# Optimization experiments

Hardware: AMD Instinct MI355X
Metric: run time of the kernel (lower is better)

## Reference

```python
import jax, jax.numpy as jnp
import numpy as np

B, C, N = 8, 768, 256
H = 12            # num_heads[0]
D = C // H        # head_dim = 64


def setup_inputs() -> dict:
    key = jax.random.key(0)
    ks = jax.random.split(key, 4)
    s = 0.02
    return {
        "x_ori": jax.random.normal(ks[0], (B, C, N), jnp.float32),
        "cross": jax.random.normal(ks[1], (B, C, N), jnp.float32),
        "W_proj": jax.random.normal(ks[2], (C, C), jnp.float32) * s,
        "b_proj": jnp.zeros((C,), jnp.float32),
        "W_dep": jax.random.normal(ks[3], (C, C), jnp.float32) * s,
        "b_dep": jnp.zeros((C,), jnp.float32),
    }


def reference(x_ori, cross, W_proj, b_proj, W_dep, b_dep):
    # x_ori, cross: [B, C, N] with channel axis factored as (head_dim D, num_heads H)
    Bn, Cn, Nn = x_ori.shape
    Nc = cross.shape[-1]
    scale = D ** (-0.5)

    # 'B (d H) N -> B d (H N)'
    x = x_ori.reshape(Bn, D, H, Nn).reshape(Bn, D, H * Nn)

    # proj over channel axis (1x1 conv): [B, C, Nc]
    cp = jnp.einsum('oc,bcn->bon', W_proj, cross) + b_proj[None, :, None]
    cp = cp.reshape(Bn, D, H, Nc).reshape(Bn, D, H * Nc)      # 'B (d H) Nc -> B d (H Nc)'

    # 'B (d H) Nc -> B (H Nc) d'
    cr = cross.reshape(Bn, D, H, Nc).transpose(0, 2, 3, 1).reshape(Bn, H * Nc, D)

    # raw attention (no softmax in original source)
    atten = jnp.einsum('bdm,bdn->bmn', x, cp) * scale          # [B, H*N, H*Nc]
    out = jnp.einsum('bmn,bnd->bmd', atten, cr)                # [B, H*N, D]

    # 'B (N H) d -> B N (H d)'  (note (num, head) grouping per source)
    out = out.reshape(Bn, Nn, H, D).reshape(Bn, Nn, H * D)

    y = out @ W_dep.T + b_dep                                  # deproj: [B, N, C]
    # skip connection (dropout is identity at eval / drop_ratio=0)
    return x_ori + y.transpose(0, 2, 1)
```

## Files before the change

kernel.cpp:

```cpp
#include <hip/hip_runtime.h>

typedef unsigned short u16;
typedef short bf16x8 __attribute__((ext_vector_type(8)));
typedef float f32x4 __attribute__((ext_vector_type(4)));

#define BB 8
#define CC 768
#define NN 256
#define HH 12
#define DD 64
#define K3 3072
#define BCN 196608
#define SCALE 0.125f
#define LDP 72

__device__ __forceinline__ u16 f2b(float f) {
    union { float f; unsigned int i; } v; v.f = f;
    unsigned int r = v.i + 0x7FFFu + ((v.i >> 16) & 1u);
    return (u16)(r >> 16);
}

__global__ __launch_bounds__(256) void k_proj(
    const float* __restrict__ Wp, const float* __restrict__ cross,
    const float* __restrict__ bp, u16* __restrict__ cp, float* __restrict__ G)
{
    __shared__ __align__(16) u16 As[64 * LDP];
    __shared__ __align__(16) u16 Bs[64 * LDP];
    __shared__ __align__(16) float T[64][68];
    const int n0 = blockIdx.x * 64;
    const int o0 = blockIdx.y * 64;
    const int b  = blockIdx.z;
    const int t = threadIdx.x;
    const int lane = t & 63, wave = t >> 6;
    const int q = lane >> 4, tx = lane & 15;
    const int wm = (wave & 1) * 32, wn = (wave >> 1) * 32;

    if (blockIdx.x == 0 && blockIdx.y == 0) {
        float4 z = {0.f, 0.f, 0.f, 0.f};
        float* Gb = G + b * 4096;
        #pragma unroll
        for (int j = 0; j < 4; ++j)
            *reinterpret_cast<float4*>(Gb + t * 4 + j * 1024) = z;
    }

    const float* crb = cross + b * BCN;
    f32x4 acc[2][2] = {};
    for (int c0 = 0; c0 < CC; c0 += 64) {
        {
            const int r = t >> 2, cq = t & 3;
            const float* src = Wp + (o0 + r) * CC + c0;
            u16* dst = As + r * LDP;
            #pragma unroll
            for (int u = 0; u < 4; ++u) {
                const int cl = (cq + 4 * u) * 4;
                float4 v = *reinterpret_cast<const float4*>(src + cl);
                ushort4 w; w.x = f2b(v.x); w.y = f2b(v.y); w.z = f2b(v.z); w.w = f2b(v.w);
                *reinterpret_cast<ushort4*>(dst + cl) = w;
            }
        }
        {
            const int r = t >> 2, fq = t & 3;
            const float* src = crb + (c0 + r) * NN + n0;
            #pragma unroll
            for (int u = 0; u < 4; ++u) {
                const int nl = (fq + 4 * u) * 4;
                float4 v = *reinterpret_cast<const float4*>(src + nl);
                T[r][nl + 0] = v.x; T[r][nl + 1] = v.y; T[r][nl + 2] = v.z; T[r][nl + 3] = v.w;
            }
        }
        __syncthreads();
        {
            const int nn = t >> 2, cq = t & 3;
            u16* dst = Bs + nn * LDP;
            #pragma unroll
            for (int u = 0; u < 4; ++u) {
                const int c4 = (cq + 4 * u) * 4;
                ushort4 w;
                w.x = f2b(T[c4 + 0][nn]); w.y = f2b(T[c4 + 1][nn]);
                w.z = f2b(T[c4 + 2][nn]); w.w = f2b(T[c4 + 3][nn]);
                *reinterpret_cast<ushort4*>(dst + c4) = w;
            }
        }
        __syncthreads();
        #pragma unroll
        for (int kk = 0; kk < 2; ++kk) {
            bf16x8 a0 = *reinterpret_cast<bf16x8*>(As + (wm + tx) * LDP + kk * 32 + q * 8);
            bf16x8 a1 = *reinterpret_cast<bf16x8*>(As + (wm + 16 + tx) * LDP + kk * 32 + q * 8);
            bf16x8 b0 = *reinterpret_cast<bf16x8*>(Bs + (wn + tx) * LDP + kk * 32 + q * 8);
            bf16x8 b1 = *reinterpret_cast<bf16x8*>(Bs + (wn + 16 + tx) * LDP + kk * 32 + q * 8);
            acc[0][0] = __builtin_amdgcn_mfma_f32_16x16x32_bf16(a0, b0, acc[0][0], 0, 0, 0);
            acc[0][1] = __builtin_amdgcn_mfma_f32_16x16x32_bf16(a0, b1, acc[0][1], 0, 0, 0);
            acc[1][0] = __builtin_amdgcn_mfma_f32_16x16x32_bf16(a1, b0, acc[1][0], 0, 0, 0);
            acc[1][1] = __builtin_amdgcn_mfma_f32_16x16x32_bf16(a1, b1, acc[1][1], 0, 0, 0);
        }
        __syncthreads();
    }
    u16* cpb = cp + b * BCN;
    #pragma unroll
    for (int i = 0; i < 2; ++i)
        #pragma unroll
        for (int j = 0; j < 2; ++j)
            #pragma unroll
            for (int r = 0; r < 4; ++r) {
                const int o = o0 + wm + i * 16 + q * 4 + r;
                const int n = n0 + wn + j * 16 + tx;
                cpb[o * NN + n] = f2b(acc[i][j][r] + bp[o]);
            }
}

__global__ __launch_bounds__(256) void k_gram(
    const float* __restrict__ cross, const u16* __restrict__ cp, float* __restrict__ G)
{
    __shared__ __align__(16) u16 As[64 * LDP];
    __shared__ __align__(16) u16 Bs[64 * LDP];
    const int kb = blockIdx.x * 64;
    const int b  = blockIdx.y;
    const int t = threadIdx.x;
    const int lane = t & 63, wave = t >> 6;
    const int q = lane >> 4, tx = lane & 15;
    const int wm = (wave & 1) * 32, wn = (wave >> 1) * 32;
    const float* crb = cross + b * BCN;
    const u16* cpb = cp + b * BCN;
    f32x4 acc[2][2] = {};
    {
        const int r = t >> 2, cq = t & 3;
        const float* src = crb + r * K3 + kb;
        u16* dst = As + r * LDP;
        #pragma unroll
        for (int u = 0; u < 4; ++u) {
            const int cl = (cq + 4 * u) * 4;
            float4 v = *reinterpret_cast<const float4*>(src + cl);
            ushort4 w; w.x = f2b(v.x); w.y = f2b(v.y); w.z = f2b(v.z); w.w = f2b(v.w);
            *reinterpret_cast<ushort4*>(dst + cl) = w;
        }
    }
    {
        const int r = t >> 3, ch = (t & 7) * 8;
        *reinterpret_cast<uint4*>(Bs + r * LDP + ch) =
            *reinterpret_cast<const uint4*>(cpb + r * K3 + kb + ch);
        *reinterpret_cast<uint4*>(Bs + (r + 32) * LDP + ch) =
            *reinterpret_cast<const uint4*>(cpb + (r + 32) * K3 + kb + ch);
    }
    __syncthreads();
    #pragma unroll
    for (int kk = 0; kk < 2; ++kk) {
        bf16x8 a0 = *reinterpret_cast<bf16x8*>(As + (wm + tx) * LDP + kk * 32 + q * 8);
        bf16x8 a1 = *reinterpret_cast<bf16x8*>(As + (wm + 16 + tx) * LDP + kk * 32 + q * 8);
        bf16x8 b0 = *reinterpret_cast<bf16x8*>(Bs + (wn + tx) * LDP + kk * 32 + q * 8);
        bf16x8 b1 = *reinterpret_cast<bf16x8*>(Bs + (wn + 16 + tx) * LDP + kk * 32 + q * 8);
        acc[0][0] = __builtin_amdgcn_mfma_f32_16x16x32_bf16(a0, b0, acc[0][0], 0, 0, 0);
        acc[0][1] = __builtin_amdgcn_mfma_f32_16x16x32_bf16(a0, b1, acc[0][1], 0, 0, 0);
        acc[1][0] = __builtin_amdgcn_mfma_f32_16x16x32_bf16(a1, b0, acc[1][0], 0, 0, 0);
        acc[1][1] = __builtin_amdgcn_mfma_f32_16x16x32_bf16(a1, b1, acc[1][1], 0, 0, 0);
    }
    float* Gb = G + b * 4096;
    #pragma unroll
    for (int i = 0; i < 2; ++i)
        #pragma unroll
        for (int j = 0; j < 2; ++j)
            #pragma unroll
            for (int r = 0; r < 4; ++r) {
                const int dd = wm + i * 16 + q * 4 + r;
                const int d  = wn + j * 16 + tx;
                atomicAdd(Gb + dd * DD + d, acc[i][j][r] * SCALE);
            }
}

__global__ __launch_bounds__(256) void k_xm(
    const float* __restrict__ x, const float* __restrict__ G, u16* __restrict__ U)
{
    __shared__ __align__(16) u16 As[64 * LDP];
    __shared__ __align__(16) u16 Bs[64 * LDP];
    __shared__ __align__(16) float T[64][68];
    const int m0 = blockIdx.x * 64;
    const int b  = blockIdx.y;
    const int h   = m0 >> 8;
    const int nn0 = m0 & 255;
    const int t = threadIdx.x;
    const int lane = t & 63, wave = t >> 6;
    const int q = lane >> 4, tx = lane & 15;
    const int wm = (wave & 1) * 32, wn = (wave >> 1) * 32;
    const float* xb = x + b * BCN;
    const float* Gb = G + b * 4096;
    f32x4 acc[2][2] = {};
    {
        const int d = t >> 2, fq = t & 3;
        const float* src = xb + (d * HH + h) * NN + nn0;
        #pragma unroll
        for (int u = 0; u < 4; ++u) {
            const int nl = (fq + 4 * u) * 4;
            float4 v = *reinterpret_cast<const float4*>(src + nl);
            T[d][nl + 0] = v.x; T[d][nl + 1] = v.y; T[d][nl + 2] = v.z; T[d][nl + 3] = v.w;
        }
    }
    {
        const int r = t >> 2, cq = t & 3;
        const float* src = Gb + r * DD;
        u16* dst = Bs + r * LDP;
        #pragma unroll
        for (int u = 0; u < 4; ++u) {
            const int cl = (cq + 4 * u) * 4;
            float4 v = *reinterpret_cast<const float4*>(src + cl);
            ushort4 w; w.x = f2b(v.x); w.y = f2b(v.y); w.z = f2b(v.z); w.w = f2b(v.w);
            *reinterpret_cast<ushort4*>(dst + cl) = w;
        }
    }
    __syncthreads();
    {
        const int nn = t >> 2, dq = t & 3;
        u16* dst = As + nn * LDP;
        #pragma unroll
        for (int u = 0; u < 4; ++u) {
            const int d4 = (dq + 4 * u) * 4;
            ushort4 w;
            w.x = f2b(T[d4 + 0][nn]); w.y = f2b(T[d4 + 1][nn]);
            w.z = f2b(T[d4 + 2][nn]); w.w = f2b(T[d4 + 3][nn]);
            *reinterpret_cast<ushort4*>(dst + d4) = w;
        }
    }
    __syncthreads();
    #pragma unroll
    for (int kk = 0; kk < 2; ++kk) {
        bf16x8 a0 = *reinterpret_cast<bf16x8*>(As + (wm + tx) * LDP + kk * 32 + q * 8);
        bf16x8 a1 = *reinterpret_cast<bf16x8*>(As + (wm + 16 + tx) * LDP + kk * 32 + q * 8);
        bf16x8 b0 = *reinterpret_cast<bf16x8*>(Bs + (wn + tx) * LDP + kk * 32 + q * 8);
        bf16x8 b1 = *reinterpret_cast<bf16x8*>(Bs + (wn + 16 + tx) * LDP + kk * 32 + q * 8);
        acc[0][0] = __builtin_amdgcn_mfma_f32_16x16x32_bf16(a0, b0, acc[0][0], 0, 0, 0);
        acc[0][1] = __builtin_amdgcn_mfma_f32_16x16x32_bf16(a0, b1, acc[0][1], 0, 0, 0);
        acc[1][0] = __builtin_amdgcn_mfma_f32_16x16x32_bf16(a1, b0, acc[1][0], 0, 0, 0);
        acc[1][1] = __builtin_amdgcn_mfma_f32_16x16x32_bf16(a1, b1, acc[1][1], 0, 0, 0);
    }
    u16* Ub = U + b * BCN;
    #pragma unroll
    for (int i = 0; i < 2; ++i)
        #pragma unroll
        for (int j = 0; j < 2; ++j)
            #pragma unroll
            for (int r = 0; r < 4; ++r) {
                const int m  = m0 + wm + i * 16 + q * 4 + r;
                const int dd = wn + j * 16 + tx;
                Ub[m * DD + dd] = f2b(acc[i][j][r]);
            }
}

__global__ __launch_bounds__(256) void k_dep(
    const float* __restrict__ Wd, const u16* __restrict__ U,
    const float* __restrict__ bd, const float* __restrict__ x, float* __restrict__ out)
{
    __shared__ __align__(16) u16 As[64 * LDP];
    __shared__ __align__(16) u16 Bs[64 * LDP];
    const int n0 = blockIdx.x * 64;
    const int o0 = blockIdx.y * 64;
    const int b  = blockIdx.z;
    const int t = threadIdx.x;
    const int lane = t & 63, wave = t >> 6;
    const int q = lane >> 4, tx = lane & 15;
    const int wm = (wave & 1) * 32, wn = (wave >> 1) * 32;
    const u16* Ub = U + b * BCN;
    f32x4 acc[2][2] = {};
    for (int c0 = 0; c0 < CC; c0 += 64) {
        {
            const int r = t >> 2, cq = t & 3;
            const float* src = Wd + (o0 + r) * CC + c0;
            u16* dst = As + r * LDP;
            #pragma unroll
            for (int u = 0; u < 4; ++u) {
                const int cl = (cq + 4 * u) * 4;
                float4 v = *reinterpret_cast<const float4*>(src + cl);
                ushort4 w; w.x = f2b(v.x); w.y = f2b(v.y); w.z = f2b(v.z); w.w = f2b(v.w);
                *reinterpret_cast<ushort4*>(dst + cl) = w;
            }
        }
        {
            const int r = t >> 3, ch = (t & 7) * 8;
            *reinterpret_cast<uint4*>(Bs + r * LDP + ch) =
                *reinterpret_cast<const uint4*>(Ub + (n0 + r) * CC + c0 + ch);
            *reinterpret_cast<uint4*>(Bs + (r + 32) * LDP + ch) =
                *reinterpret_cast<const uint4*>(Ub + (n0 + r + 32) * CC + c0 + ch);
        }
        __syncthreads();
        #pragma unroll
        for (int kk = 0; kk < 2; ++kk) {
            bf16x8 a0 = *reinterpret_cast<bf16x8*>(As + (wm + tx) * LDP + kk * 32 + q * 8);
            bf16x8 a1 = *reinterpret_cast<bf16x8*>(As + (wm + 16 + tx) * LDP + kk * 32 + q * 8);
            bf16x8 b0 = *reinterpret_cast<bf16x8*>(Bs + (wn + tx) * LDP + kk * 32 + q * 8);
            bf16x8 b1 = *reinterpret_cast<bf16x8*>(Bs + (wn + 16 + tx) * LDP + kk * 32 + q * 8);
            acc[0][0] = __builtin_amdgcn_mfma_f32_16x16x32_bf16(a0, b0, acc[0][0], 0, 0, 0);
            acc[0][1] = __builtin_amdgcn_mfma_f32_16x16x32_bf16(a0, b1, acc[0][1], 0, 0, 0);
            acc[1][0] = __builtin_amdgcn_mfma_f32_16x16x32_bf16(a1, b0, acc[1][0], 0, 0, 0);
            acc[1][1] = __builtin_amdgcn_mfma_f32_16x16x32_bf16(a1, b1, acc[1][1], 0, 0, 0);
        }
        __syncthreads();
    }
    #pragma unroll
    for (int i = 0; i < 2; ++i)
        #pragma unroll
        for (int j = 0; j < 2; ++j)
            #pragma unroll
            for (int r = 0; r < 4; ++r) {
                const int o = o0 + wm + i * 16 + q * 4 + r;
                const int n = n0 + wn + j * 16 + tx;
                const int idx = b * BCN + o * NN + n;
                out[idx] = acc[i][j][r] + bd[o] + x[idx];
            }
}

extern "C" void kernel_launch(void* const* d_in, const int* in_sizes, int n_in,
                              void* d_out, int out_size, void* d_ws, size_t ws_size,
                              hipStream_t stream) {
    const float* x_ori = (const float*)d_in[0];
    const float* cross = (const float*)d_in[1];
    const float* Wp    = (const float*)d_in[2];
    const float* bp    = (const float*)d_in[3];
    const float* Wd    = (const float*)d_in[4];
    const float* bd    = (const float*)d_in[5];
    float* out = (float*)d_out;

    u16*   cp = (u16*)d_ws;
    u16*   U  = (u16*)d_ws;
    float* G  = (float*)((char*)d_ws + (size_t)BB * BCN * sizeof(u16));

    k_proj<<<dim3(4, 12, BB), 256, 0, stream>>>(Wp, cross, bp, cp, G);
    k_gram<<<dim3(48, BB), 256, 0, stream>>>(cross, cp, G);
    k_xm  <<<dim3(48, BB), 256, 0, stream>>>(x_ori, G, U);
    k_dep <<<dim3(4, 12, BB), 256, 0, stream>>>(Wd, U, bd, x_ori, out);
}
```

Measured before the change: 124.8 us.

## Reassociate Gram via cross self-covariance and split-K deproj with atomics

Replaces the projection-then-Gram pipeline with a per-batch cross covariance S = cross·crossᵀ (768x768 with K=256), then forms the head Gram by contracting W_proj against S, adding the bias term through row sums of cross. The x transpose and bf16 conversion is folded into the first kernel, and the output is initialised with x + b_dep inside the xm kernel. Deproj is split along K into two halves that atomically accumulate into the output. This trades the K=768 projection GEMM for a smaller S GEMM plus a strided W_proj GEMM, but adds a 9.4MB bf16 S intermediate and float atomics on the output.

```diff
diff --git a/kernel.cpp b/kernel.cpp
--- a/kernel.cpp
+++ b/kernel.cpp
@@ -9,8 +9,8 @@
 #define NN 256
 #define HH 12
 #define DD 64
-#define K3 3072
 #define BCN 196608
+#define SWS 589824
 #define SCALE 0.125f
 #define LDP 72
 
@@ -20,66 +20,157 @@
     return (u16)(r >> 16);
 }
 
-__global__ __launch_bounds__(256) void k_proj(
-    const float* __restrict__ Wp, const float* __restrict__ cross,
-    const float* __restrict__ bp, u16* __restrict__ cp, float* __restrict__ G)
+
+__global__ __launch_bounds__(256) void k_S(
+    const float* __restrict__ cross, const float* __restrict__ x,
+    u16* __restrict__ S, u16* __restrict__ xT,
+    float* __restrict__ G, float* __restrict__ R)
 {
-    __shared__ __align__(16) u16 As[64 * LDP];
-    __shared__ __align__(16) u16 Bs[64 * LDP];
-    __shared__ __align__(16) float T[64][68];
-    const int n0 = blockIdx.x * 64;
-    const int o0 = blockIdx.y * 64;
-    const int b  = blockIdx.z;
-    const int t = threadIdx.x;
+    __shared__ __align__(16) u16 SMEM[2 * 64 * LDP];
+    u16* As = SMEM;
+    u16* Bs = SMEM + 64 * LDP;
+    float (*T)[68] = reinterpret_cast<float(*)[68]>(SMEM);
+    const int b = blockIdx.y, blk = blockIdx.x, t = threadIdx.x;
     const int lane = t & 63, wave = t >> 6;
     const int q = lane >> 4, tx = lane & 15;
     const int wm = (wave & 1) * 32, wn = (wave >> 1) * 32;
 
-    if (blockIdx.x == 0 && blockIdx.y == 0) {
-        float4 z = {0.f, 0.f, 0.f, 0.f};
-        float* Gb = G + b * 4096;
-        #pragma unroll
-        for (int j = 0; j < 4; ++j)
-            *reinterpret_cast<float4*>(Gb + t * 4 + j * 1024) = z;
-    }
-
-    const float* crb = cross + b * BCN;
+    if (blk < 144) {
+        const int r0 = (blk / 12) * 64, c0 = (blk % 12) * 64;
+        const float* crb = cross + b * BCN;
+        f32x4 acc[2][2] = {};
+        for (int k4 = 0; k4 < 4; ++k4) {
+            const int nk = k4 * 64;
+            {
+                const int r = t >> 2, q4 = t & 3;
+                const float* sa = crb + (r0 + r) * NN + nk;
+                const float* sb = crb + (c0 + r) * NN + nk;
+                u16* da = As + r * LDP;
+                u16* db = Bs + r * LDP;
+                #pragma unroll
+                for (int u = 0; u < 4; ++u) {
+                    const int cl = (q4 + 4 * u) * 4;
+                    float4 va = *reinterpret_cast<const float4*>(sa + cl);
+                    float4 vb = *reinterpret_cast<const float4*>(sb + cl);
+                    ushort4 wa, wb;
+                    wa.x = f2b(va.x); wa.y = f2b(va.y); wa.z = f2b(va.z); wa.w = f2b(va.w);
+                    wb.x = f2b(vb.x); wb.y = f2b(vb.y); wb.z = f2b(vb.z); wb.w = f2b(vb.w);
+                    *reinterpret_cast<ushort4*>(da + cl) = wa;
+                    *reinterpret_cast<ushort4*>(db + cl) = wb;
+                }
+            }
+            __syncthreads();
+            #pragma unroll
+            for (int kk = 0; kk < 2; ++kk) {
+                bf16x8 a0 = *reinterpret_cast<bf16x8*>(As + (wm + tx) * LDP + kk * 32 + q * 8);
+                bf16x8 a1 = *reinterpret_cast<bf16x8*>(As + (wm + 16 + tx) * LDP + kk * 32 + q * 8);
+                bf16x8 b0 = *reinterpret_cast<bf16x8*>(Bs + (wn + tx) * LDP + kk * 32 + q * 8);
+                bf16x8 b1 = *reinterpret_cast<bf16x8*>(Bs + (wn + 16 + tx) * LDP + kk * 32 + q * 8);
+                acc[0][0] = __builtin_amdgcn_mfma_f32_16x16x32_bf16(a0, b0, acc[0][0], 0, 0, 0);
+                acc[0][1] = __builtin_amdgcn_mfma_f32_16x16x32_bf16(a0, b1, acc[0][1], 0, 0, 0);
+                acc[1][0] = __builtin_amdgcn_mfma_f32_16x16x32_bf16(a1, b0, acc[1][0], 0, 0, 0);
+                acc[1][1] = __builtin_amdgcn_mfma_f32_16x16x32_bf16(a1, b1, acc[1][1], 0, 0, 0);
+            }
+            __syncthreads();
+        }
+        u16* Sb = S + b * SWS;
+        #pragma unroll
+        for (int i = 0; i < 2; ++i)
+            #pragma unroll
+            for (int j = 0; j < 2; ++j)
+                #pragma unroll
+                for (int r = 0; r < 4; ++r) {
+                    const int row = r0 + wm + i * 16 + q * 4 + r;
+                    const int col = c0 + wn + j * 16 + tx;
+                    Sb[row * CC + col] = f2b(acc[i][j][r]);
+                }
+        if (blk == 0) {
+            float4 z = {0.f, 0.f, 0.f, 0.f};
+            float* Gb = G + b * 4096;
+            #pragma unroll
+            for (int u = 0; u < 4; ++u)
+                *reinterpret_cast<float4*>(Gb + t * 16 + u * 4) = z;
+        }
+        if (r0 == c0) {
+            float* Rp = (float*)As;
+            const int row = t >> 2, seg = t & 3;
+            const float* src = crb + (r0 + row) * NN + seg * 64;
+            float s = 0.f;
+            #pragma unroll
+            for (int u = 0; u < 16; ++u) {
+                float4 v = *reinterpret_cast<const float4*>(src + u * 4);
+                s += v.x + v.y + v.z + v.w;
+            }
+            Rp[t] = s;
+            __syncthreads();
+            if (t < 64)
+                R[b * CC + r0 + t] = Rp[t * 4] + Rp[t * 4 + 1] + Rp[t * 4 + 2] + Rp[t * 4 + 3];
+        }
+    } else {
+        const int idx = blk - 144;
+        const int m0 = idx * 64, h = m0 >> 8, nn0 = m0 & 255;
+        const float* xb = x + b * BCN;
+        {
+            const int d = t >> 2, fq = t & 3;
+            const float* src = xb + (d * HH + h) * NN + nn0;
+            #pragma unroll
+            for (int u = 0; u < 4; ++u) {
+                const int nl = (fq + 4 * u) * 4;
+                float4 v = *reinterpret_cast<const float4*>(src + nl);
+                T[d][nl + 0] = v.x; T[d][nl + 1] = v.y; T[d][nl + 2] = v.z; T[d][nl + 3] = v.w;
+            }
+        }
+        __syncthreads();
+        {
+            const int nn = t >> 2, dq = t & 3;
+            u16* dst = xT + b * BCN + (m0 + nn) * DD;
+            #pragma unroll
+            for (int u = 0; u < 4; ++u) {
+                const int d4 = (dq + 4 * u) * 4;
+                ushort4 w;
+                w.x = f2b(T[d4 + 0][nn]); w.y = f2b(T[d4 + 1][nn]);
+                w.z = f2b(T[d4 + 2][nn]); w.w = f2b(T[d4 + 3][nn]);
+                *reinterpret_cast<ushort4*>(dst + d4) = w;
+            }
+        }
+    }
+}
+
+__global__ __launch_bounds__(256) void k_g(
+    const float* __restrict__ Wp, const u16* __restrict__ S,
+    const float* __restrict__ bp, const float* __restrict__ R,
+    float* __restrict__ G)
+{
+    __shared__ __align__(16) u16 SMEM[2 * 64 * LDP];
+    u16* As = SMEM;
+    u16* Bs = SMEM + 64 * LDP;
+    const int b = blockIdx.y, kc = blockIdx.x, t = threadIdx.x;
+    const int j = kc >> 1, cb = (kc & 1) * 384;
+    const int lane = t & 63, wave = t >> 6;
+    const int q = lane >> 4, tx = lane & 15;
+    const int wm = (wave & 1) * 32, wn = (wave >> 1) * 32;
+    const u16* Sb = S + b * SWS;
     f32x4 acc[2][2] = {};
-    for (int c0 = 0; c0 < CC; c0 += 64) {
-        {
-            const int r = t >> 2, cq = t & 3;
-            const float* src = Wp + (o0 + r) * CC + c0;
+    for (int ii = 0; ii < 6; ++ii) {
+        const int c0 = cb + ii * 64;
+        {
+            const int r = t >> 2, q4 = t & 3;
+            const float* src = Wp + (r * HH + j) * CC + c0;
             u16* dst = As + r * LDP;
             #pragma unroll
             for (int u = 0; u < 4; ++u) {
-                const int cl = (cq + 4 * u) * 4;
+                const int cl = (q4 + 4 * u) * 4;
                 float4 v = *reinterpret_cast<const float4*>(src + cl);
                 ushort4 w; w.x = f2b(v.x); w.y = f2b(v.y); w.z = f2b(v.z); w.w = f2b(v.w);
                 *reinterpret_cast<ushort4*>(dst + cl) = w;
             }
         }
         {
-            const int r = t >> 2, fq = t & 3;
-            const float* src = crb + (c0 + r) * NN + n0;
-            #pragma unroll
-            for (int u = 0; u < 4; ++u) {
-                const int nl = (fq + 4 * u) * 4;
-                float4 v = *reinterpret_cast<const float4*>(src + nl);
-                T[r][nl + 0] = v.x; T[r][nl + 1] = v.y; T[r][nl + 2] = v.z; T[r][nl + 3] = v.w;
-            }
-        }
-        __syncthreads();
-        {
-            const int nn = t >> 2, cq = t & 3;
-            u16* dst = Bs + nn * LDP;
-            #pragma unroll
-            for (int u = 0; u < 4; ++u) {
-                const int c4 = (cq + 4 * u) * 4;
-                ushort4 w;
-                w.x = f2b(T[c4 + 0][nn]); w.y = f2b(T[c4 + 1][nn]);
-                w.z = f2b(T[c4 + 2][nn]); w.w = f2b(T[c4 + 3][nn]);
-                *reinterpret_cast<ushort4*>(dst + c4) = w;
-            }
+            const int r = t >> 3, ch = (t & 7) * 8;
+            *reinterpret_cast<uint4*>(Bs + r * LDP + ch) =
+                *reinterpret_cast<const uint4*>(Sb + (r * HH + j) * CC + c0 + ch);
+            *reinterpret_cast<uint4*>(Bs + (r + 32) * LDP + ch) =
+                *reinterpret_cast<const uint4*>(Sb + ((r + 32) * HH + j) * CC + c0 + ch);
         }
         __syncthreads();
         #pragma unroll
@@ -95,188 +186,80 @@
         }
         __syncthreads();
     }
-    u16* cpb = cp + b * BCN;
-    #pragma unroll
-    for (int i = 0; i < 2; ++i)
-        #pragma unroll
-        for (int j = 0; j < 2; ++j)
-            #pragma unroll
-            for (int r = 0; r < 4; ++r) {
-                const int o = o0 + wm + i * 16 + q * 4 + r;
-                const int n = n0 + wn + j * 16 + tx;
-                cpb[o * NN + n] = f2b(acc[i][j][r] + bp[o]);
-            }
-}
-
-__global__ __launch_bounds__(256) void k_gram(
-    const float* __restrict__ cross, const u16* __restrict__ cp, float* __restrict__ G)
+    float* Gb = G + b * 4096;
+    if (kc == 0) {
+        float* bpf = (float*)As;
+        float* Rf  = bpf + CC;
+        #pragma unroll
+        for (int u = 0; u < 3; ++u) {
+            const int idx = t + u * 256;
+            bpf[idx] = bp[idx];
+            Rf[idx]  = R[b * CC + idx];
+        }
+        __syncthreads();
+        #pragma unroll
+        for (int i = 0; i < 2; ++i)
+            #pragma unroll
+            for (int j2 = 0; j2 < 2; ++j2)
+                #pragma unroll
+                for (int r = 0; r < 4; ++r) {
+                    const int dI  = wm + i * 16 + q * 4 + r;
+                    const int ddI = wn + j2 * 16 + tx;
+                    float bias = 0.f;
+                    #pragma unroll
+                    for (int jj = 0; jj < HH; ++jj)
+                        bias += bpf[dI * HH + jj] * Rf[ddI * HH + jj];
+                    atomicAdd(Gb + ddI * DD + dI, SCALE * (acc[i][j2][r] + bias));
+                }
+    } else {
+        #pragma unroll
+        for (int i = 0; i < 2; ++i)
+            #pragma unroll
+            for (int j2 = 0; j2 < 2; ++j2)
+                #pragma unroll
+                for (int r = 0; r < 4; ++r) {
+                    const int dI  = wm + i * 16 + q * 4 + r;
+                    const int ddI = wn + j2 * 16 + tx;
+                    atomicAdd(Gb + ddI * DD + dI, SCALE * acc[i][j2][r]);
+                }
+    }
+}
+
+__global__ __launch_bounds__(256) void k_xm2(
+    const u16* __restrict__ xT, const float* __restrict__ G,
+    const float* __restrict__ x, const float* __restrict__ bd,
+    u16* __restrict__ U, float* __restrict__ out)
 {
-    __shared__ __align__(16) u16 As[64 * LDP];
-    __shared__ __align__(16) u16 Bs[64 * LDP];
-    const int kb = blockIdx.x * 64;
-    const int b  = blockIdx.y;
-    const int t = threadIdx.x;
-    const int lane = t & 63, wave = t >> 6;
-    const int q = lane >> 4, tx = lane & 15;
-    const int wm = (wave & 1) * 32, wn = (wave >> 1) * 32;
-    const float* crb = cross + b * BCN;
-    const u16* cpb = cp + b * BCN;
-    f32x4 acc[2][2] = {};
-    {
-        const int r = t >> 2, cq = t & 3;
-        const float* src = crb + r * K3 + kb;
-        u16* dst = As + r * LDP;
-        #pragma unroll
-        for (int u = 0; u < 4; ++u) {
-            const int cl = (cq + 4 * u) * 4;
-            float4 v = *reinterpret_cast<const float4*>(src + cl);
-            ushort4 w; w.x = f2b(v.x); w.y = f2b(v.y); w.z = f2b(v.z); w.w = f2b(v.w);
-            *reinterpret_cast<ushort4*>(dst + cl) = w;
-        }
-    }
-    {
-        const int r = t >> 3, ch = (t & 7) * 8;
-        *reinterpret_cast<uint4*>(Bs + r * LDP + ch) =
-            *reinterpret_cast<const uint4*>(cpb + r * K3 + kb + ch);
-        *reinterpret_cast<uint4*>(Bs + (r + 32) * LDP + ch) =
-            *reinterpret_cast<const uint4*>(cpb + (r + 32) * K3 + kb + ch);
-    }
-    __syncthreads();
-    #pragma unroll
-    for (int kk = 0; kk < 2; ++kk) {
-        bf16x8 a0 = *reinterpret_cast<bf16x8*>(As + (wm + tx) * LDP + kk * 32 + q * 8);
-        bf16x8 a1 = *reinterpret_cast<bf16x8*>(As + (wm + 16 + tx) * LDP + kk * 32 + q * 8);
-        bf16x8 b0 = *reinterpret_cast<bf16x8*>(Bs + (wn + tx) * LDP + kk * 32 + q * 8);
-        bf16x8 b1 = *reinterpret_cast<bf16x8*>(Bs + (wn + 16 + tx) * LDP + kk * 32 + q * 8);
-        acc[0][0] = __builtin_amdgcn_mfma_f32_16x16x32_bf16(a0, b0, acc[0][0], 0, 0, 0);
-        acc[0][1] = __builtin_amdgcn_mfma_f32_16x16x32_bf16(a0, b1, acc[0][1], 0, 0, 0);
-        acc[1][0] = __builtin_amdgcn_mfma_f32_16x16x32_bf16(a1, b0, acc[1][0], 0, 0, 0);
-        acc[1][1] = __builtin_amdgcn_mfma_f32_16x16x32_bf16(a1, b1, acc[1][1], 0, 0, 0);
-    }
-    float* Gb = G + b * 4096;
-    #pragma unroll
-    for (int i = 0; i < 2; ++i)
-        #pragma unroll
-        for (int j = 0; j < 2; ++j)
-            #pragma unroll
-            for (int r = 0; r < 4; ++r) {
-                const int dd = wm + i * 16 + q * 4 + r;
-                const int d  = wn + j * 16 + tx;
-                atomicAdd(Gb + dd * DD + d, acc[i][j][r] * SCALE);
-            }
-}
-
-__global__ __launch_bounds__(256) void k_xm(
-    const float* __restrict__ x, const float* __restrict__ G, u16* __restrict__ U)
-{
-    __shared__ __align__(16) u16 As[64 * LDP];
-    __shared__ __align__(16) u16 Bs[64 * LDP];
-    __shared__ __align__(16) float T[64][68];
-    const int m0 = blockIdx.x * 64;
-    const int b  = blockIdx.y;
-    const int h   = m0 >> 8;
-    const int nn0 = m0 & 255;
-    const int t = threadIdx.x;
-    const int lane = t & 63, wave = t >> 6;
-    const int q = lane >> 4, tx = lane & 15;
-    const int wm = (wave & 1) * 32, wn = (wave >> 1) * 32;
-    const float* xb = x + b * BCN;
-    const float* Gb = G + b * 4096;
-    f32x4 acc[2][2] = {};
-    {
-        const int d = t >> 2, fq = t & 3;
-        const float* src = xb + (d * HH + h) * NN + nn0;
-        #pragma unroll
-        for (int u = 0; u < 4; ++u) {
-            const int nl = (fq + 4 * u) * 4;
-            float4 v = *reinterpret_cast<const float4*>(src + nl);
-            T[d][nl + 0] = v.x; T[d][nl + 1] = v.y; T[d][nl + 2] = v.z; T[d][nl + 3] = v.w;
-        }
-    }
-    {
-        const int r = t >> 2, cq = t & 3;
-        const float* src = Gb + r * DD;
-        u16* dst = Bs + r * LDP;
-        #pragma unroll
-        for (int u = 0; u < 4; ++u) {
-            const int cl = (cq + 4 * u) * 4;
-            float4 v = *reinterpret_cast<const float4*>(src + cl);
-            ushort4 w; w.x = f2b(v.x); w.y = f2b(v.y); w.z = f2b(v.z); w.w = f2b(v.w);
-            *reinterpret_cast<ushort4*>(dst + cl) = w;
-        }
-    }
-    __syncthreads();
-    {
-        const int nn = t >> 2, dq = t & 3;
-        u16* dst = As + nn * LDP;
-        #pragma unroll
-        for (int u = 0; u < 4; ++u) {
-            const int d4 = (dq + 4 * u) * 4;
-            ushort4 w;
-            w.x = f2b(T[d4 + 0][nn]); w.y = f2b(T[d4 + 1][nn]);
-            w.z = f2b(T[d4 + 2][nn]); w.w = f2b(T[d4 + 3][nn]);
-            *reinterpret_cast<ushort4*>(dst + d4) = w;
-        }
-    }
-    __syncthreads();
-    #pragma unroll
-    for (int kk = 0; kk < 2; ++kk) {
-        bf16x8 a0 = *reinterpret_cast<bf16x8*>(As + (wm + tx) * LDP + kk * 32 + q * 8);
-        bf16x8 a1 = *reinterpret_cast<bf16x8*>(As + (wm + 16 + tx) * LDP + kk * 32 + q * 8);
-        bf16x8 b0 = *reinterpret_cast<bf16x8*>(Bs + (wn + tx) * LDP + kk * 32 + q * 8);
-        bf16x8 b1 = *reinterpret_cast<bf16x8*>(Bs + (wn + 16 + tx) * LDP + kk * 32 + q * 8);
-        acc[0][0] = __builtin_amdgcn_mfma_f32_16x16x32_bf16(a0, b0, acc[0][0], 0, 0, 0);
-        acc[0][1] = __builtin_amdgcn_mfma_f32_16x16x32_bf16(a0, b1, acc[0][1], 0, 0, 0);
-        acc[1][0] = __builtin_amdgcn_mfma_f32_16x16x32_bf16(a1, b0, acc[1][0], 0, 0, 0);
-        acc[1][1] = __builtin_amdgcn_mfma_f32_16x16x32_bf16(a1, b1, acc[1][1], 0, 0, 0);
-    }
-    u16* Ub = U + b * BCN;
-    #pragma unroll
-    for (int i = 0; i < 2; ++i)
-        #pragma unroll
-        for (int j = 0; j < 2; ++j)
-            #pragma unroll
-            for (int r = 0; r < 4; ++r) {
-                const int m  = m0 + wm + i * 16 + q * 4 + r;
-                const int dd = wn + j * 16 + tx;
-                Ub[m * DD + dd] = f2b(acc[i][j][r]);
-            }
-}
-
-__global__ __launch_bounds__(256) void k_dep(
-    const float* __restrict__ Wd, const u16* __restrict__ U,
-    const float* __restrict__ bd, const float* __restrict__ x, float* __restrict__ out)
-{
-    __shared__ __align__(16) u16 As[64 * LDP];
-    __shared__ __align__(16) u16 Bs[64 * LDP];
-    const int n0 = blockIdx.x * 64;
-    const int o0 = blockIdx.y * 64;
-    const int b  = blockIdx.z;
-    const int t = threadIdx.x;
-    const int lane = t & 63, wave = t >> 6;
-    const int q = lane >> 4, tx = lane & 15;
-    const int wm = (wave & 1) * 32, wn = (wave >> 1) * 32;
-    const u16* Ub = U + b * BCN;
-    f32x4 acc[2][2] = {};
-    for (int c0 = 0; c0 < CC; c0 += 64) {
-        {
-            const int r = t >> 2, cq = t & 3;
-            const float* src = Wd + (o0 + r) * CC + c0;
-            u16* dst = As + r * LDP;
-            #pragma unroll
-            for (int u = 0; u < 4; ++u) {
-                const int cl = (cq + 4 * u) * 4;
+    __shared__ __align__(16) u16 SMEM[2 * 64 * LDP];
+    u16* As = SMEM;
+    u16* Bs = SMEM + 64 * LDP;
+    const int b = blockIdx.y, blk = blockIdx.x, t = threadIdx.x;
+    if (blk < 48) {
+        const int m0 = blk * 64;
+        const int lane = t & 63, wave = t >> 6;
+        const int q = lane >> 4, tx = lane & 15;
+        const int wm = (wave & 1) * 32, wn = (wave >> 1) * 32;
+        const u16* xTb = xT + b * BCN;
+        const float* Gb = G + b * 4096;
+        f32x4 acc[2][2] = {};
+        {
+            const int r = t >> 3, ch = (t & 7) * 8;
+            *reinterpret_cast<uint4*>(As + r * LDP + ch) =
+                *reinterpret_cast<const uint4*>(xTb + (m0 + r) * DD + ch);
+            *reinterpret_cast<uint4*>(As + (r + 32) * LDP + ch) =
+                *reinterpret_cast<const uint4*>(xTb + (m0 + r + 32) * DD + ch);
+        }
+        {
+            const int r = t >> 2, q4 = t & 3;
+            const float* src = Gb + r * DD;
+            u16* dst = Bs + r * LDP;
+            #pragma unroll
+            for (int u = 0; u < 4; ++u) {
+                const int cl = (q4 + 4 * u) * 4;
                 float4 v = *reinterpret_cast<const float4*>(src + cl);
                 ushort4 w; w.x = f2b(v.x); w.y = f2b(v.y); w.z = f2b(v.z); w.w = f2b(v.w);
                 *reinterpret_cast<ushort4*>(dst + cl) = w;
             }
-        }
-        {
-            const int r = t >> 3, ch = (t & 7) * 8;
-            *reinterpret_cast<uint4*>(Bs + r * LDP + ch) =
-                *reinterpret_cast<const uint4*>(Ub + (n0 + r) * CC + c0 + ch);
-            *reinterpret_cast<uint4*>(Bs + (r + 32) * LDP + ch) =
-                *reinterpret_cast<const uint4*>(Ub + (n0 + r + 32) * CC + c0 + ch);
         }
         __syncthreads();
         #pragma unroll
@@ -290,6 +273,80 @@
             acc[1][0] = __builtin_amdgcn_mfma_f32_16x16x32_bf16(a1, b0, acc[1][0], 0, 0, 0);
             acc[1][1] = __builtin_amdgcn_mfma_f32_16x16x32_bf16(a1, b1, acc[1][1], 0, 0, 0);
         }
+        u16* Ub = U + b * BCN;
+        #pragma unroll
+        for (int i = 0; i < 2; ++i)
+            #pragma unroll
+            for (int j = 0; j < 2; ++j)
+                #pragma unroll
+                for (int r = 0; r < 4; ++r) {
+                    const int m  = m0 + wm + i * 16 + q * 4 + r;
+                    const int dd = wn + j * 16 + tx;
+                    Ub[m * DD + dd] = f2b(acc[i][j][r]);
+                }
+    } else {
+        const int idx = blk - 48;
+        const int base = b * BCN + idx * 4096 + t * 16;
+        #pragma unroll
+        for (int u = 0; u < 4; ++u) {
+            const int off = idx * 4096 + t * 16 + u * 4;
+            const int o = off >> 8;
+            float4 v = *reinterpret_cast<const float4*>(x + base + u * 4);
+            const float bb = bd[o];
+            v.x += bb; v.y += bb; v.z += bb; v.w += bb;
+            *reinterpret_cast<float4*>(out + base + u * 4) = v;
+        }
+    }
+}
+
+__global__ __launch_bounds__(256) void k_dep(
+    const float* __restrict__ Wd, const u16* __restrict__ U, float* __restrict__ out)
+{
+    __shared__ __align__(16) u16 As[64 * LDP];
+    __shared__ __align__(16) u16 Bs[64 * LDP];
+    const int n0 = blockIdx.x * 64;
+    const int o0 = blockIdx.y * 64;
+    const int b  = blockIdx.z >> 1;
+    const int cb = (blockIdx.z & 1) * 384;
+    const int t = threadIdx.x;
+    const int lane = t & 63, wave = t >> 6;
+    const int q = lane >> 4, tx = lane & 15;
+    const int wm = (wave & 1) * 32, wn = (wave >> 1) * 32;
+    const u16* Ub = U + b * BCN;
+    f32x4 acc[2][2] = {};
+    for (int ii = 0; ii < 6; ++ii) {
+        const int c0 = cb + ii * 64;
+        {
+            const int r = t >> 2, q4 = t & 3;
+            const float* src = Wd + (o0 + r) * CC + c0;
+            u16* dst = As + r * LDP;
+            #pragma unroll
+            for (int u = 0; u < 4; ++u) {
+                const int cl = (q4 + 4 * u) * 4;
+                float4 v = *reinterpret_cast<const float4*>(src + cl);
+                ushort4 w; w.x = f2b(v.x); w.y = f2b(v.y); w.z = f2b(v.z); w.w = f2b(v.w);
+                *reinterpret_cast<ushort4*>(dst + cl) = w;
+            }
+        }
+        {
+            const int r = t >> 3, ch = (t & 7) * 8;
+            *reinterpret_cast<uint4*>(Bs + r * LDP + ch) =
+                *reinterpret_cast<const uint4*>(Ub + (n0 + r) * CC + c0 + ch);
+            *reinterpret_cast<uint4*>(Bs + (r + 32) * LDP + ch) =
+                *reinterpret_cast<const uint4*>(Ub + (n0 + r + 32) * CC + c0 + ch);
+        }
+        __syncthreads();
+        #pragma unroll
+        for (int kk = 0; kk < 2; ++kk) {
+            bf16x8 a0 = *reinterpret_cast<bf16x8*>(As + (wm + tx) * LDP + kk * 32 + q * 8);
+            bf16x8 a1 = *reinterpret_cast<bf16x8*>(As + (wm + 16 + tx) * LDP + kk * 32 + q * 8);
+            bf16x8 b0 = *reinterpret_cast<bf16x8*>(Bs + (wn + tx) * LDP + kk * 32 + q * 8);
+            bf16x8 b1 = *reinterpret_cast<bf16x8*>(Bs + (wn + 16 + tx) * LDP + kk * 32 + q * 8);
+            acc[0][0] = __builtin_amdgcn_mfma_f32_16x16x32_bf16(a0, b0, acc[0][0], 0, 0, 0);
+            acc[0][1] = __builtin_amdgcn_mfma_f32_16x16x32_bf16(a0, b1, acc[0][1], 0, 0, 0);
+            acc[1][0] = __builtin_amdgcn_mfma_f32_16x16x32_bf16(a1, b0, acc[1][0], 0, 0, 0);
+            acc[1][1] = __builtin_amdgcn_mfma_f32_16x16x32_bf16(a1, b1, acc[1][1], 0, 0, 0);
+        }
         __syncthreads();
     }
     #pragma unroll
@@ -300,8 +357,7 @@
             for (int r = 0; r < 4; ++r) {
                 const int o = o0 + wm + i * 16 + q * 4 + r;
                 const int n = n0 + wn + j * 16 + tx;
-                const int idx = b * BCN + o * NN + n;
-                out[idx] = acc[i][j][r] + bd[o] + x[idx];
+                atomicAdd(out + b * BCN + o * NN + n, acc[i][j][r]);
             }
 }
 
@@ -316,12 +372,15 @@
     const float* bd    = (const float*)d_in[5];
     float* out = (float*)d_out;
 
-    u16*   cp = (u16*)d_ws;
-    u16*   U  = (u16*)d_ws;
-    float* G  = (float*)((char*)d_ws + (size_t)BB * BCN * sizeof(u16));
-
-    k_proj<<<dim3(4, 12, BB), 256, 0, stream>>>(Wp, cross, bp, cp, G);
-    k_gram<<<dim3(48, BB), 256, 0, stream>>>(cross, cp, G);
-    k_xm  <<<dim3(48, BB), 256, 0, stream>>>(x_ori, G, U);
-    k_dep <<<dim3(4, 12, BB), 256, 0, stream>>>(Wd, U, bd, x_ori, out);
-}
+    char* ws = (char*)d_ws;
+    u16*   S  = (u16*)ws;
+    u16*   xT = (u16*)(ws + 9437184);
+    u16*   U  = (u16*)(ws + 12582912);
+    float* G  = (float*)(ws + 15728640);
+    float* R  = (float*)(ws + 15859712);
+
+    k_S  <<<dim3(192, BB), 256, 0, stream>>>(cross, x_ori, S, xT, G, R);
+    k_g  <<<dim3(24, BB), 256, 0, stream>>>(Wp, S, bp, R, G);
+    k_xm2<<<dim3(96, BB), 256, 0, stream>>>(xT, G, x_ori, bd, U, out);
+    k_dep<<<dim3(4, 12, 16), 256, 0, stream>>>(Wd, U, out);
+}
```

Result: no change. 126.2 us (+1.1%).
